# Optimization experiments

Hardware: AMD Instinct MI355X
Metric: run time of the kernel (lower is better)

Reference implementation:

```python
import jax, jax.numpy as jnp
import numpy as np

N_HEADS = 8
OUT_DIM = 64
LEAKY_SLOPE = 0.2


def setup_inputs() -> dict:
    key = jax.random.key(0)
    k1, k2, k3 = jax.random.split(key, 3)
    N, IN_DIM = 4096, 256
    x = jax.random.normal(k1, (N, IN_DIM), dtype=jnp.float32)
    # nn.Linear(in_dim, out_dim*n_heads, bias=False): weight shape (out*heads, in)
    W = jax.random.normal(k2, (OUT_DIM * N_HEADS, IN_DIM), dtype=jnp.float32) * (1.0 / np.sqrt(IN_DIM))
    # attention vector, xavier-ish scale
    attn = jax.random.normal(k3, (1, N_HEADS, 2 * OUT_DIM), dtype=jnp.float32) * 0.1
    return {"x": x, "W": W, "attn": attn}


def reference(x, W, attn):
    N = x.shape[0]
    # Wx: (N, H, D)
    Wx = (x @ W.T).reshape(N, N_HEADS, OUT_DIM)
    # The torch code concats src/tgt then dots with attn; this decomposes exactly:
    # e[i,j,h] = leaky_relu( Wx[i,h]·a_src[h] + Wx[j,h]·a_tgt[h] )
    a_src = attn[0, :, :OUT_DIM]   # (H, D)
    a_tgt = attn[0, :, OUT_DIM:]   # (H, D)
    s = jnp.einsum('nhd,hd->nh', Wx, a_src)  # (N, H) score of row index (src)
    t = jnp.einsum('nhd,hd->nh', Wx, a_tgt)  # (N, H) score of col index (tgt)
    e = jax.nn.leaky_relu(s[:, None, :] + t[None, :, :], LEAKY_SLOPE)  # (N, N, H)
    a = jax.nn.softmax(e, axis=1)  # softmax over dim=1 (neighbors j)
    # out[i,h,d] = sum_j a[i,j,h] * Wx[j,h,d]
    out = jnp.einsum('ijh,jhd->ihd', a, Wx)
    return out.reshape(N, N_HEADS * OUT_DIM)  # concat=True
```

## Files before the change

kernel.cpp:

```cpp
#include <hip/hip_runtime.h>
#include <hip/hip_bf16.h>

#define NN 4096
#define KD 256
#define NH 8
#define DD 64
#define HD 512
#define SLOPE 0.2f
#define NSLICE 8
#define SLEN 512

__global__ __launch_bounds__(256) void gemm_st(const float* __restrict__ x,
                                               const float* __restrict__ W,
                                               const float* __restrict__ attn,
                                               float* __restrict__ Wx,
                                               float* __restrict__ sH,
                                               float* __restrict__ tH) {
    const int h  = blockIdx.x;
    const int bn = h * 64;
    const int bm = blockIdx.y * 64;
    __shared__ float As[32][68];
    __shared__ float Bs[32][68];
    const int tid = threadIdx.x;
    const int tx = tid & 15, ty = tid >> 4;
    const int srow = tid >> 2;
    const int skq  = (tid & 3) * 8;
    float acc[4][4] = {};
    for (int k0 = 0; k0 < KD; k0 += 32) {
        float4 a0 = *(const float4*)&x[(bm + srow) * KD + k0 + skq];
        float4 a1 = *(const float4*)&x[(bm + srow) * KD + k0 + skq + 4];
        float4 b0 = *(const float4*)&W[(bn + srow) * KD + k0 + skq];
        float4 b1 = *(const float4*)&W[(bn + srow) * KD + k0 + skq + 4];
        __syncthreads();
        As[skq + 0][srow] = a0.x; As[skq + 1][srow] = a0.y;
        As[skq + 2][srow] = a0.z; As[skq + 3][srow] = a0.w;
        As[skq + 4][srow] = a1.x; As[skq + 5][srow] = a1.y;
        As[skq + 6][srow] = a1.z; As[skq + 7][srow] = a1.w;
        Bs[skq + 0][srow] = b0.x; Bs[skq + 1][srow] = b0.y;
        Bs[skq + 2][srow] = b0.z; Bs[skq + 3][srow] = b0.w;
        Bs[skq + 4][srow] = b1.x; Bs[skq + 5][srow] = b1.y;
        Bs[skq + 6][srow] = b1.z; Bs[skq + 7][srow] = b1.w;
        __syncthreads();
#pragma unroll
        for (int kk = 0; kk < 32; ++kk) {
            float4 a = *(const float4*)&As[kk][ty * 4];
            float4 b = *(const float4*)&Bs[kk][tx * 4];
            acc[0][0] += a.x * b.x; acc[0][1] += a.x * b.y; acc[0][2] += a.x * b.z; acc[0][3] += a.x * b.w;
            acc[1][0] += a.y * b.x; acc[1][1] += a.y * b.y; acc[1][2] += a.y * b.z; acc[1][3] += a.y * b.w;
            acc[2][0] += a.z * b.x; acc[2][1] += a.z * b.y; acc[2][2] += a.z * b.z; acc[2][3] += a.z * b.w;
            acc[3][0] += a.w * b.x; acc[3][1] += a.w * b.y; acc[3][2] += a.w * b.z; acc[3][3] += a.w * b.w;
        }
    }
#pragma unroll
    for (int m = 0; m < 4; ++m)
        *(float4*)&Wx[(bm + ty * 4 + m) * HD + bn + tx * 4] = *(const float4*)&acc[m][0];
    float4 as4 = *(const float4*)&attn[h * 128 + tx * 4];
    float4 at4 = *(const float4*)&attn[h * 128 + 64 + tx * 4];
#pragma unroll
    for (int m = 0; m < 4; ++m) {
        float s = acc[m][0] * as4.x + acc[m][1] * as4.y + acc[m][2] * as4.z + acc[m][3] * as4.w;
        float t = acc[m][0] * at4.x + acc[m][1] * at4.y + acc[m][2] * at4.z + acc[m][3] * at4.w;
#pragma unroll
        for (int off = 1; off < 16; off <<= 1) {
            s += __shfl_xor(s, off, 16);
            t += __shfl_xor(t, off, 16);
        }
        if (tx == 0) {
            sH[h * NN + bm + ty * 4 + m] = s;
            tH[h * NN + bm + ty * 4 + m] = t;
        }
    }
}

__global__ __launch_bounds__(256) void count_partial(const float* __restrict__ tH,
                                                     const float* __restrict__ sH,
                                                     unsigned short* __restrict__ partialR,
                                                     unsigned short* __restrict__ partialC) {
    const int h = blockIdx.y;
    const int slice = blockIdx.z;
    const int jb = blockIdx.x;
    const int j = jb * 256 + threadIdx.x;
    __shared__ float tl[SLEN];
    for (int p = threadIdx.x; p < SLEN; p += 256) tl[p] = tH[h * NN + slice * SLEN + p];
    __syncthreads();
    const float myT  = tH[h * NN + j];
    const float negS = -sH[h * NN + j];
    const float4* tl4 = (const float4*)tl;
    int r = 0, cs = 0;
    if (slice == (jb >> 1)) {
        const int pbase = slice * SLEN;
#pragma unroll 4
        for (int p4 = 0; p4 < SLEN / 4; ++p4) {
            float4 v = tl4[p4];
            int p = pbase + p4 * 4;
            r += (v.x < myT) | ((v.x == myT) & ((p + 0) < j));
            r += (v.y < myT) | ((v.y == myT) & ((p + 1) < j));
            r += (v.z < myT) | ((v.z == myT) & ((p + 2) < j));
            r += (v.w < myT) | ((v.w == myT) & ((p + 3) < j));
            cs += (v.x <= negS) + (v.y <= negS) + (v.z <= negS) + (v.w <= negS);
        }
    } else if (slice < (jb >> 1)) {
#pragma unroll 4
        for (int p4 = 0; p4 < SLEN / 4; ++p4) {
            float4 v = tl4[p4];
            r  += (v.x <= myT) + (v.y <= myT) + (v.z <= myT) + (v.w <= myT);
            cs += (v.x <= negS) + (v.y <= negS) + (v.z <= negS) + (v.w <= negS);
        }
    } else {
#pragma unroll 4
        for (int p4 = 0; p4 < SLEN / 4; ++p4) {
            float4 v = tl4[p4];
            r  += (v.x < myT) + (v.y < myT) + (v.z < myT) + (v.w < myT);
            cs += (v.x <= negS) + (v.y <= negS) + (v.z <= negS) + (v.w <= negS);
        }
    }
    partialR[(h * NSLICE + slice) * NN + j] = (unsigned short)r;
    partialC[(h * NSLICE + slice) * NN + j] = (unsigned short)cs;
}

__global__ __launch_bounds__(256) void scatter_kernel(const float* __restrict__ tH,
                                                      const unsigned short* __restrict__ partialR,
                                                      const unsigned short* __restrict__ partialC,
                                                      int* __restrict__ sortedIdx,
                                                      float* __restrict__ expT,
                                                      float* __restrict__ expT2,
                                                      int* __restrict__ cIdx) {
    const int h = blockIdx.y;
    const int j = blockIdx.x * 256 + threadIdx.x;
    int r = 0, cs = 0;
#pragma unroll
    for (int s = 0; s < NSLICE; ++s) {
        r  += partialR[(h * NSLICE + s) * NN + j];
        cs += partialC[(h * NSLICE + s) * NN + j];
    }
    const float myT = tH[h * NN + j];
    sortedIdx[h * NN + r] = j;
    expT[h * NN + r]      = expf(myT);
    expT2[h * NN + r]     = expf(SLOPE * myT);
    cIdx[h * NN + j]      = cs;
}

__global__ __launch_bounds__(256) void local_prefix(const float* __restrict__ Wx,
                                                    const int* __restrict__ sortedIdx,
                                                    const float* __restrict__ expT,
                                                    const float* __restrict__ expT2,
                                                    float* __restrict__ localW,
                                                    float* __restrict__ localW2,
                                                    float* __restrict__ chunkTotW,
                                                    float* __restrict__ chunkTotW2,
                                                    float* __restrict__ localZ,
                                                    float* __restrict__ localZ2,
                                                    float* __restrict__ chunkZtot,
                                                    float* __restrict__ chunkZtot2) {
    const int c = blockIdx.x, h = blockIdx.y;
    const int tid = threadIdx.x;
    const int wid = tid >> 6, d = tid & 63;
    const int base = h * NN + c * 64;
    __shared__ float sums[4][64], sums2[4][64];
    float run = 0.f, run2 = 0.f;
    float ex[16], ex2[16];
#pragma unroll
    for (int kk = 0; kk < 16; ++kk) {
        int k = wid * 16 + kk;
        int j = sortedIdx[base + k];
        float w  = expT[base + k];
        float w2 = expT2[base + k];
        float v = Wx[j * HD + h * DD + d];
        ex[kk]  = run;  run  += w  * v;
        ex2[kk] = run2; run2 += w2 * v;
    }
    sums[wid][d] = run; sums2[wid][d] = run2;
    __syncthreads();
    float off = 0.f, off2 = 0.f;
    for (int w = 0; w < 4; ++w) {
        if (w < wid) { off += sums[w][d]; off2 += sums2[w][d]; }
    }
#pragma unroll
    for (int kk = 0; kk < 16; ++kk) {
        int k = wid * 16 + kk;
        localW [(h * NN + c * 64 + k) * 64 + d] = ex[kk]  + off;
        localW2[(h * NN + c * 64 + k) * 64 + d] = ex2[kk] + off2;
    }
    if (wid == 3) {
        chunkTotW [(h * 64 + c) * 64 + d] = off  + run;
        chunkTotW2[(h * 64 + c) * 64 + d] = off2 + run2;
    }
    if (wid == 0) {
        float z0 = expT[base + d];
        float z = z0;
#pragma unroll
        for (int o = 1; o < 64; o <<= 1) { float n = __shfl_up(z, o, 64); if (d >= o) z += n; }
        localZ[h * NN + c * 64 + d] = z - z0;
        if (d == 63) chunkZtot[h * 64 + c] = z;
    } else if (wid == 1) {
        float z0 = expT2[base + d];
        float z = z0;
#pragma unroll
        for (int o = 1; o < 64; o <<= 1) { float n = __shfl_up(z, o, 64); if (d >= o) z += n; }
        localZ2[h * NN + c * 64 + d] = z - z0;
        if (d == 63) chunkZtot2[h * 64 + c] = z;
    }
}

__global__ __launch_bounds__(256) void chunk_scan(float* __restrict__ chunkTotW,
                                                  float* __restrict__ chunkTotW2,
                                                  float* __restrict__ chunkZtot,
                                                  float* __restrict__ chunkZtot2,
                                                  float* __restrict__ totW,
                                                  float* __restrict__ totW2,
                                                  float* __restrict__ Ztot,
                                                  float* __restrict__ Ztot2) {
    const int h = blockIdx.x;
    const int tid = threadIdx.x;
    const int lane = tid & 63;
    __shared__ float cw[64 * 64];
    __shared__ float cw2[64 * 64];
    __shared__ float zb[64], zb2[64];
#pragma unroll
    for (int it = 0; it < 16; ++it) {
        int lin = it * 256 + tid;
        cw[lin]  = chunkTotW [h * 4096 + lin];
        cw2[lin] = chunkTotW2[h * 4096 + lin];
    }
    if (tid >= 128 && tid < 192) zb[lane]  = chunkZtot [h * 64 + lane];
    if (tid >= 192)              zb2[lane] = chunkZtot2[h * 64 + lane];
    __syncthreads();
    if (tid < 64) {
        float acc = 0.f;
        for (int c = 0; c < 64; ++c) { int idx = c * 64 + tid; float t = cw[idx]; cw[idx] = acc; acc += t; }
        totW[h * 64 + tid] = acc;
    } else if (tid < 128) {
        int d = tid - 64;
        float acc = 0.f;
        for (int c = 0; c < 64; ++c) { int idx = c * 64 + d; float t = cw2[idx]; cw2[idx] = acc; acc += t; }
        totW2[h * 64 + d] = acc;
    } else if (tid < 192) {
        float z0 = zb[lane];
        float z = z0;
#pragma unroll
        for (int o = 1; o < 64; o <<= 1) { float n = __shfl_up(z, o, 64); if (lane >= o) z += n; }
        chunkZtot[h * 64 + lane] = z - z0;
        if (lane == 63) Ztot[h] = z;
    } else {
        float z0 = zb2[lane];
        float z = z0;
#pragma unroll
        for (int o = 1; o < 64; o <<= 1) { float n = __shfl_up(z, o, 64); if (lane >= o) z += n; }
        chunkZtot2[h * 64 + lane] = z - z0;
        if (lane == 63) Ztot2[h] = z;
    }
    __syncthreads();
#pragma unroll
    for (int it = 0; it < 16; ++it) {
        int lin = it * 256 + tid;
        chunkTotW [h * 4096 + lin] = cw[lin];
        chunkTotW2[h * 4096 + lin] = cw2[lin];
    }
}

__global__ __launch_bounds__(256) void out_kernel(const float* __restrict__ sH,
                                                  const int* __restrict__ cIdx,
                                                  const float* __restrict__ localW,
                                                  const float* __restrict__ localW2,
                                                  const float* __restrict__ chunkTotW,
                                                  const float* __restrict__ chunkTotW2,
                                                  const float* __restrict__ localZ,
                                                  const float* __restrict__ localZ2,
                                                  const float* __restrict__ chunkZtot,
                                                  const float* __restrict__ chunkZtot2,
                                                  const float* __restrict__ totW,
                                                  const float* __restrict__ totW2,
                                                  const float* __restrict__ Ztot,
                                                  const float* __restrict__ Ztot2,
                                                  float* __restrict__ out) {
    const int h = blockIdx.y;
    const int i = blockIdx.x * 4 + (threadIdx.x >> 6);
    const int d = threadIdx.x & 63;
    const float sv = sH[h * NN + i];
    const int c = cIdx[h * NN + i];
    const float es  = expf(sv);
    const float es2 = expf(SLOPE * sv);
    float wpos, wneg, zp, zn;
    if (c == NN) {
        wpos = 0.f; zp = 0.f;
        wneg = totW2[h * 64 + d];
        zn   = Ztot2[h];
    } else {
        float pw  = localW [(h * NN + c) * 64 + d] + chunkTotW [(h * 64 + (c >> 6)) * 64 + d];
        float pw2 = localW2[(h * NN + c) * 64 + d] + chunkTotW2[(h * 64 + (c >> 6)) * 64 + d];
        wpos = totW[h * 64 + d] - pw;
        wneg = pw2;
        float pz  = localZ [h * NN + c] + chunkZtot [h * 64 + (c >> 6)];
        float pz2 = localZ2[h * NN + c] + chunkZtot2[h * 64 + (c >> 6)];
        zp = Ztot[h] - pz;
        zn = pz2;
    }
    out[i * HD + h * DD + d] = (es * wpos + es2 * wneg) / (es * zp + es2 * zn);
}

extern "C" void kernel_launch(void* const* d_in, const int* in_sizes, int n_in,
                              void* d_out, int out_size, void* d_ws, size_t ws_size,
                              hipStream_t stream) {
    const float* x    = (const float*)d_in[0];
    const float* W    = (const float*)d_in[1];
    const float* attn = (const float*)d_in[2];
    float* out = (float*)d_out;

    float* ws = (float*)d_ws;
    size_t o = 0;
    float* Wx        = ws + o; o += (size_t)NN * HD;
    float* sH        = ws + o; o += (size_t)NH * NN;
    float* tH        = ws + o; o += (size_t)NH * NN;
    float* expT      = ws + o; o += (size_t)NH * NN;
    float* expT2     = ws + o; o += (size_t)NH * NN;
    int*   sortedIdx = (int*)(ws + o); o += (size_t)NH * NN;
    int*   cIdx      = (int*)(ws + o); o += (size_t)NH * NN;
    float* localZ    = ws + o; o += (size_t)NH * NN;
    float* localZ2   = ws + o; o += (size_t)NH * NN;
    float* chunkTotW  = ws + o; o += (size_t)NH * 64 * 64;
    float* chunkTotW2 = ws + o; o += (size_t)NH * 64 * 64;
    float* chunkZtot  = ws + o; o += (size_t)NH * 64;
    float* chunkZtot2 = ws + o; o += (size_t)NH * 64;
    float* totW   = ws + o; o += (size_t)NH * 64;
    float* totW2  = ws + o; o += (size_t)NH * 64;
    float* Ztot   = ws + o; o += 64;
    float* Ztot2  = ws + o; o += 64;
    float* localW  = ws + o; o += (size_t)NH * NN * 64;
    float* localW2 = ws + o; o += (size_t)NH * NN * 64;
    unsigned short* partialR = (unsigned short*)localW;
    unsigned short* partialC = (unsigned short*)localW2;

    gemm_st<<<dim3(NH, NN / 64), dim3(256), 0, stream>>>(x, W, attn, Wx, sH, tH);
    count_partial<<<dim3(NN / 256, NH, NSLICE), dim3(256), 0, stream>>>(tH, sH, partialR, partialC);
    scatter_kernel<<<dim3(NN / 256, NH), dim3(256), 0, stream>>>(tH, partialR, partialC, sortedIdx, expT, expT2, cIdx);
    local_prefix<<<dim3(64, NH), dim3(256), 0, stream>>>(Wx, sortedIdx, expT, expT2, localW, localW2,
                                                         chunkTotW, chunkTotW2, localZ, localZ2, chunkZtot, chunkZtot2);
    chunk_scan<<<dim3(NH), dim3(256), 0, stream>>>(chunkTotW, chunkTotW2, chunkZtot, chunkZtot2,
                                                   totW, totW2, Ztot, Ztot2);
    out_kernel<<<dim3(NN / 4, NH), dim3(256), 0, stream>>>(sH, cIdx, localW, localW2, chunkTotW, chunkTotW2,
                                                           localZ, localZ2, chunkZtot, chunkZtot2,
                                                           totW, totW2, Ztot, Ztot2, out);
}
```

Baseline: 72.97 us.

## Fuse rank counting and scatter into one kernel with in-block slice reduction

Merges the sliced rank/count kernel and the scatter kernel into a single kernel in which four waves each scan a 1024-element quarter of the t scores directly from global memory, then reduce the partial counts in shared memory and scatter. This removes one launch and the round trip of the ushort partial arrays. The GEMM grid is also flattened to 1D with a remapped tile order, which changes block scheduling and cache locality. In exchange the counting kernel has fewer blocks (512 instead of 1024), more serial work per thread, and no shared-memory staging of t.

```diff
diff --git a/kernel.cpp b/kernel.cpp
--- a/kernel.cpp
+++ b/kernel.cpp
@@ -7,8 +7,6 @@
 #define DD 64
 #define HD 512
 #define SLOPE 0.2f
-#define NSLICE 8
-#define SLEN 512
 
 __global__ __launch_bounds__(256) void gemm_st(const float* __restrict__ x,
                                                const float* __restrict__ W,
@@ -16,9 +14,11 @@
                                                float* __restrict__ Wx,
                                                float* __restrict__ sH,
                                                float* __restrict__ tH) {
-    const int h  = blockIdx.x;
+    const int b = blockIdx.x;
+    const int bmTile = (b & 7) * 8 + ((b >> 3) & 7);
+    const int h = b >> 6;
     const int bn = h * 64;
-    const int bm = blockIdx.y * 64;
+    const int bm = bmTile * 64;
     __shared__ float As[32][68];
     __shared__ float Bs[32][68];
     const int tid = threadIdx.x;
@@ -44,11 +44,11 @@
 #pragma unroll
         for (int kk = 0; kk < 32; ++kk) {
             float4 a = *(const float4*)&As[kk][ty * 4];
-            float4 b = *(const float4*)&Bs[kk][tx * 4];
-            acc[0][0] += a.x * b.x; acc[0][1] += a.x * b.y; acc[0][2] += a.x * b.z; acc[0][3] += a.x * b.w;
-            acc[1][0] += a.y * b.x; acc[1][1] += a.y * b.y; acc[1][2] += a.y * b.z; acc[1][3] += a.y * b.w;
-            acc[2][0] += a.z * b.x; acc[2][1] += a.z * b.y; acc[2][2] += a.z * b.z; acc[2][3] += a.z * b.w;
-            acc[3][0] += a.w * b.x; acc[3][1] += a.w * b.y; acc[3][2] += a.w * b.z; acc[3][3] += a.w * b.w;
+            float4 bb = *(const float4*)&Bs[kk][tx * 4];
+            acc[0][0] += a.x * bb.x; acc[0][1] += a.x * bb.y; acc[0][2] += a.x * bb.z; acc[0][3] += a.x * bb.w;
+            acc[1][0] += a.y * bb.x; acc[1][1] += a.y * bb.y; acc[1][2] += a.y * bb.z; acc[1][3] += a.y * bb.w;
+            acc[2][0] += a.z * bb.x; acc[2][1] += a.z * bb.y; acc[2][2] += a.z * bb.z; acc[2][3] += a.z * bb.w;
+            acc[3][0] += a.w * bb.x; acc[3][1] += a.w * bb.y; acc[3][2] += a.w * bb.z; acc[3][3] += a.w * bb.w;
         }
     }
 #pragma unroll
@@ -72,26 +72,42 @@
     }
 }
 
-__global__ __launch_bounds__(256) void count_partial(const float* __restrict__ tH,
+__global__ __launch_bounds__(256) void count_scatter(const float* __restrict__ tH,
                                                      const float* __restrict__ sH,
-                                                     unsigned short* __restrict__ partialR,
-                                                     unsigned short* __restrict__ partialC) {
-    const int h = blockIdx.y;
-    const int slice = blockIdx.z;
-    const int jb = blockIdx.x;
-    const int j = jb * 256 + threadIdx.x;
-    __shared__ float tl[SLEN];
-    for (int p = threadIdx.x; p < SLEN; p += 256) tl[p] = tH[h * NN + slice * SLEN + p];
-    __syncthreads();
+                                                     int* __restrict__ sortedIdx,
+                                                     float* __restrict__ expT,
+                                                     float* __restrict__ expT2,
+                                                     int* __restrict__ cIdx) {
+    const int h  = blockIdx.y;
+    const int jg = blockIdx.x;
+    const int tid = threadIdx.x;
+    const int w  = tid >> 6;
+    const int jj = tid & 63;
+    const int j  = jg * 64 + jj;
+    const int qj = jg >> 4;
     const float myT  = tH[h * NN + j];
     const float negS = -sH[h * NN + j];
-    const float4* tl4 = (const float4*)tl;
+    const float4* t4 = (const float4*)&tH[h * NN + w * 1024];
     int r = 0, cs = 0;
-    if (slice == (jb >> 1)) {
-        const int pbase = slice * SLEN;
+    if (w < qj) {
+#pragma unroll 8
+        for (int p4 = 0; p4 < 256; ++p4) {
+            float4 v = t4[p4];
+            r  += (v.x <= myT) + (v.y <= myT) + (v.z <= myT) + (v.w <= myT);
+            cs += (v.x <= negS) + (v.y <= negS) + (v.z <= negS) + (v.w <= negS);
+        }
+    } else if (w > qj) {
+#pragma unroll 8
+        for (int p4 = 0; p4 < 256; ++p4) {
+            float4 v = t4[p4];
+            r  += (v.x < myT) + (v.y < myT) + (v.z < myT) + (v.w < myT);
+            cs += (v.x <= negS) + (v.y <= negS) + (v.z <= negS) + (v.w <= negS);
+        }
+    } else {
+        const int pbase = w * 1024;
 #pragma unroll 4
-        for (int p4 = 0; p4 < SLEN / 4; ++p4) {
-            float4 v = tl4[p4];
+        for (int p4 = 0; p4 < 256; ++p4) {
+            float4 v = t4[p4];
             int p = pbase + p4 * 4;
             r += (v.x < myT) | ((v.x == myT) & ((p + 0) < j));
             r += (v.y < myT) | ((v.y == myT) & ((p + 1) < j));
@@ -99,45 +115,20 @@
             r += (v.w < myT) | ((v.w == myT) & ((p + 3) < j));
             cs += (v.x <= negS) + (v.y <= negS) + (v.z <= negS) + (v.w <= negS);
         }
-    } else if (slice < (jb >> 1)) {
-#pragma unroll 4
-        for (int p4 = 0; p4 < SLEN / 4; ++p4) {
-            float4 v = tl4[p4];
-            r  += (v.x <= myT) + (v.y <= myT) + (v.z <= myT) + (v.w <= myT);
-            cs += (v.x <= negS) + (v.y <= negS) + (v.z <= negS) + (v.w <= negS);
-        }
-    } else {
-#pragma unroll 4
-        for (int p4 = 0; p4 < SLEN / 4; ++p4) {
-            float4 v = tl4[p4];
-            r  += (v.x < myT) + (v.y < myT) + (v.z < myT) + (v.w < myT);
-            cs += (v.x <= negS) + (v.y <= negS) + (v.z <= negS) + (v.w <= negS);
-        }
-    }
-    partialR[(h * NSLICE + slice) * NN + j] = (unsigned short)r;
-    partialC[(h * NSLICE + slice) * NN + j] = (unsigned short)cs;
-}
-
-__global__ __launch_bounds__(256) void scatter_kernel(const float* __restrict__ tH,
-                                                      const unsigned short* __restrict__ partialR,
-                                                      const unsigned short* __restrict__ partialC,
-                                                      int* __restrict__ sortedIdx,
-                                                      float* __restrict__ expT,
-                                                      float* __restrict__ expT2,
-                                                      int* __restrict__ cIdx) {
-    const int h = blockIdx.y;
-    const int j = blockIdx.x * 256 + threadIdx.x;
-    int r = 0, cs = 0;
-#pragma unroll
-    for (int s = 0; s < NSLICE; ++s) {
-        r  += partialR[(h * NSLICE + s) * NN + j];
-        cs += partialC[(h * NSLICE + s) * NN + j];
-    }
-    const float myT = tH[h * NN + j];
-    sortedIdx[h * NN + r] = j;
-    expT[h * NN + r]      = expf(myT);
-    expT2[h * NN + r]     = expf(SLOPE * myT);
-    cIdx[h * NN + j]      = cs;
+    }
+    __shared__ int rsum[4][64], csum[4][64];
+    rsum[w][jj] = r; csum[w][jj] = cs;
+    __syncthreads();
+    if (tid < 64) {
+        const int jt = jg * 64 + tid;
+        int R  = rsum[0][tid] + rsum[1][tid] + rsum[2][tid] + rsum[3][tid];
+        int CS = csum[0][tid] + csum[1][tid] + csum[2][tid] + csum[3][tid];
+        const float tv = tH[h * NN + jt];
+        sortedIdx[h * NN + R] = jt;
+        expT [h * NN + R] = expf(tv);
+        expT2[h * NN + R] = expf(SLOPE * tv);
+        cIdx[h * NN + jt] = CS;
+    }
 }
 
 __global__ __launch_bounds__(256) void local_prefix(const float* __restrict__ Wx,
@@ -172,9 +163,8 @@
     sums[wid][d] = run; sums2[wid][d] = run2;
     __syncthreads();
     float off = 0.f, off2 = 0.f;
-    for (int w = 0; w < 4; ++w) {
+    for (int w = 0; w < 4; ++w)
         if (w < wid) { off += sums[w][d]; off2 += sums2[w][d]; }
-    }
 #pragma unroll
     for (int kk = 0; kk < 16; ++kk) {
         int k = wid * 16 + kk;
@@ -327,12 +317,9 @@
     float* Ztot2  = ws + o; o += 64;
     float* localW  = ws + o; o += (size_t)NH * NN * 64;
     float* localW2 = ws + o; o += (size_t)NH * NN * 64;
-    unsigned short* partialR = (unsigned short*)localW;
-    unsigned short* partialC = (unsigned short*)localW2;
-
-    gemm_st<<<dim3(NH, NN / 64), dim3(256), 0, stream>>>(x, W, attn, Wx, sH, tH);
-    count_partial<<<dim3(NN / 256, NH, NSLICE), dim3(256), 0, stream>>>(tH, sH, partialR, partialC);
-    scatter_kernel<<<dim3(NN / 256, NH), dim3(256), 0, stream>>>(tH, partialR, partialC, sortedIdx, expT, expT2, cIdx);
+
+    gemm_st<<<dim3(512), dim3(256), 0, stream>>>(x, W, attn, Wx, sH, tH);
+    count_scatter<<<dim3(64, NH), dim3(256), 0, stream>>>(tH, sH, sortedIdx, expT, expT2, cIdx);
     local_prefix<<<dim3(64, NH), dim3(256), 0, stream>>>(Wx, sortedIdx, expT, expT2, localW, localW2,
                                                          chunkTotW, chunkTotW2, localZ, localZ2, chunkZtot, chunkZtot2);
     chunk_scan<<<dim3(NH), dim3(256), 0, stream>>>(chunkTotW, chunkTotW2, chunkZtot, chunkZtot2,
```

Result: slower. 83.72 us (+14.7%).
